# Kernel tuning notes

Hardware: AMD Instinct MI355X
Metric: run time of the kernel (lower is better)

## Reference

```python
import jax, jax.numpy as jnp
import numpy as np


def graph_conv(x, W, b, src, dst, n_nodes):
    """DGL GraphConv, norm='both', activation=relu.
    Pre-scale by out-degree^-1/2 of src, project (in>out so project first),
    sum-aggregate over edges, post-scale by in-degree^-1/2 of dst."""
    ones = jnp.ones(src.shape[0], dtype=x.dtype)
    deg_out = jax.ops.segment_sum(ones, src, num_segments=n_nodes)
    deg_in = jax.ops.segment_sum(ones, dst, num_segments=n_nodes)
    norm_src = jnp.clip(deg_out, 1.0, None) ** -0.5  # [N]
    norm_dst = jnp.clip(deg_in, 1.0, None) ** -0.5   # [N]
    h = x * norm_src[:, None]
    h = h @ W  # project first since in_feats > out_feats
    # message passing: gather src features, scatter-add into dst
    agg = jax.ops.segment_sum(h[src], dst, num_segments=n_nodes)  # [N, out]
    agg = agg * norm_dst[:, None]
    return jax.nn.relu(agg + b)


def setup_inputs() -> dict:
    key = jax.random.key(0)
    ks = jax.random.split(key, 6)
    N, E, D_IN, D_HID = 50000, 800000, 1024, 256
    x = jax.random.normal(ks[0], (N, D_IN), dtype=jnp.float32)
    src = jax.random.randint(ks[1], (E,), 0, N)
    dst = jax.random.randint(ks[2], (E,), 0, N)
    # Glorot-style init for weights
    W1 = jax.random.normal(ks[3], (D_IN, D_HID), dtype=jnp.float32) * (1.0 / np.sqrt(D_IN))
    b1 = jnp.zeros((D_HID,), dtype=jnp.float32)
    W2 = jax.random.normal(ks[4], (D_HID, 1), dtype=jnp.float32) * (1.0 / np.sqrt(D_HID))
    b2 = jnp.zeros((1,), dtype=jnp.float32)
    return {"x": x, "src": src, "dst": dst, "W1": W1, "b1": b1, "W2": W2, "b2": b2, "n_nodes": N}


def reference(x, src, dst, W1, b1, W2, b2, n_nodes):
    h = graph_conv(x, W1, b1, src, dst, n_nodes)   # [N, 256]
    out = graph_conv(h, W2, b2, src, dst, n_nodes)  # [N, 1]
    return out
```

## Files before the change

kernel.cpp:

```cpp
#include <hip/hip_runtime.h>
#include <hip/hip_bf16.h>

typedef __attribute__((ext_vector_type(8))) short bf16x8;
typedef __attribute__((ext_vector_type(4))) float f32x4;

static __device__ __forceinline__ short f2bf(float f) {
    unsigned u = __float_as_uint(f);
    unsigned r = (u + 0x7FFFu + ((u >> 16) & 1u)) >> 16;
    return (short)(unsigned short)r;
}
static __device__ __forceinline__ float bf2f(short s) {
    return __uint_as_float(((unsigned)(unsigned short)s) << 16);
}

static __device__ __forceinline__ void gload16(const void* g, void* l) {
    __builtin_amdgcn_global_load_lds((const __attribute__((address_space(1))) unsigned int*)g,
                                     (__attribute__((address_space(3))) unsigned int*)l, 16, 0, 0);
}

static __device__ __forceinline__ bf16x8 cvt8(const f32x4 lo, const f32x4 hi) {
    __hip_bfloat162 p0 = __float22bfloat162_rn(make_float2(lo[0], lo[1]));
    __hip_bfloat162 p1 = __float22bfloat162_rn(make_float2(lo[2], lo[3]));
    __hip_bfloat162 p2 = __float22bfloat162_rn(make_float2(hi[0], hi[1]));
    __hip_bfloat162 p3 = __float22bfloat162_rn(make_float2(hi[2], hi[3]));
    short2 s0 = *(short2*)&p0, s1 = *(short2*)&p1, s2 = *(short2*)&p2, s3 = *(short2*)&p3;
    bf16x8 r = {s0.x, s0.y, s1.x, s1.y, s2.x, s2.y, s3.x, s3.y};
    return r;
}

__global__ void deg_kernel(const int* __restrict__ src, const int* __restrict__ dst,
                           int* __restrict__ deg_out, int* __restrict__ deg_in, int E) {
    int e = blockIdx.x * blockDim.x + threadIdx.x;
    if (e < E) {
        atomicAdd(&deg_out[src[e]], 1);
        atomicAdd(&deg_in[dst[e]], 1);
    }
}

__global__ void norm_kernel(const int* __restrict__ deg_out, const int* __restrict__ deg_in,
                            float* __restrict__ ns, float* __restrict__ nd, int N) {
    int i = blockIdx.x * blockDim.x + threadIdx.x;
    if (i < N) {
        ns[i] = rsqrtf((float)max(deg_out[i], 1));
        nd[i] = rsqrtf((float)max(deg_in[i], 1));
    }
}

__global__ void scan_part1(const int* __restrict__ deg, int* __restrict__ bsum, int N) {
    __shared__ int red[256];
    int i = blockIdx.x * 256 + threadIdx.x;
    red[threadIdx.x] = (i < N) ? deg[i] : 0;
    __syncthreads();
    for (int off = 128; off > 0; off >>= 1) {
        if (threadIdx.x < off) red[threadIdx.x] += red[threadIdx.x + off];
        __syncthreads();
    }
    if (threadIdx.x == 0) bsum[blockIdx.x] = red[0];
}

__global__ void scan_part2(const int* __restrict__ bsum, int* __restrict__ bsum_ex, int NB,
                           int* __restrict__ offsets, int N, int E) {
    __shared__ int s[256];
    int t = threadIdx.x;
    int v = (t < NB) ? bsum[t] : 0;
    s[t] = v;
    __syncthreads();
    for (int off = 1; off < 256; off <<= 1) {
        int u = (t >= off) ? s[t - off] : 0;
        __syncthreads();
        s[t] += u;
        __syncthreads();
    }
    bsum_ex[t] = s[t] - v;
    if (t == 0) offsets[N] = E;
}

__global__ void scan_part3(const int* __restrict__ deg, const int* __restrict__ bsum_ex,
                           int* __restrict__ offsets, int N) {
    __shared__ int s[256];
    int t = threadIdx.x, i = blockIdx.x * 256 + t;
    int v = (i < N) ? deg[i] : 0;
    s[t] = v;
    __syncthreads();
    for (int off = 1; off < 256; off <<= 1) {
        int u = (t >= off) ? s[t - off] : 0;
        __syncthreads();
        s[t] += u;
        __syncthreads();
    }
    if (i < N) offsets[i] = bsum_ex[blockIdx.x] + s[t] - v;
}

__global__ void scatter_kernel(const int* __restrict__ src, const int* __restrict__ dst,
                               const int* __restrict__ offsets, int* __restrict__ cursor,
                               int* __restrict__ bucket, int E) {
    int e = blockIdx.x * blockDim.x + threadIdx.x;
    if (e < E) {
        int d = dst[e];
        int p = atomicAdd(&cursor[d], 1);
        bucket[offsets[d] + p] = src[e];
    }
}

__global__ __launch_bounds__(1024) void transpose_w1(const float* __restrict__ W1,
                                                     short* __restrict__ Wt) {
    __shared__ short tile[32][33];
    int k0 = blockIdx.x * 32, n0 = blockIdx.y * 32;
    int tx = threadIdx.x & 31, ty = threadIdx.x >> 5;
    tile[ty][tx] = f2bf(W1[(size_t)(k0 + ty) * 256 + (n0 + tx)]);
    __syncthreads();
    Wt[(size_t)(n0 + ty) * 1024 + (k0 + tx)] = tile[tx][ty];
}

#define BM 128
#define BN 128
#define BK 32
#define CSTR 136

union SMem {
    struct {
        float A[BM * BK];
        short B[BN * BK];
    } s;
    short C[BM * CSTR];
};

__global__ __launch_bounds__(256, 3) void gemm1_kernel(const float* __restrict__ x,
                                                       const short* __restrict__ Wt,
                                                       const float* __restrict__ norm_src,
                                                       short* __restrict__ hb, int M) {
    __shared__ __align__(16) SMem sm;
    __shared__ float ns_lds[BM];
    const int tid  = threadIdx.x;
    const int lane = tid & 63;
    const int wave = tid >> 6;
    const int quad = lane >> 4;
    const int mrow = lane & 15;
    const int wm = (wave >> 1) * 64;
    const int wn = (wave & 1) * 64;
    const int bm = blockIdx.x * BM;
    const int bn = blockIdx.y * BN;

    if (tid < BM) ns_lds[tid] = norm_src[min(bm + tid, M - 1)];

    f32x4 acc[4][4] = {};

    const int aL_r = lane >> 3;
    const int aL_c = (lane & 7) ^ (aL_r & 7);
    const int bL_r = lane >> 2;
    const int bL_c = (lane & 3) ^ ((lane >> 3) & 3);

    for (int k0 = 0; k0 < 1024; k0 += BK) {
#pragma unroll
        for (int i = 0; i < 4; i++) {
            int rowbase = wave * 32 + i * 8;
            int r = rowbase + aL_r;
            if (bm + r < M)
                gload16(x + (size_t)(bm + r) * 1024 + k0 + aL_c * 4, &sm.s.A[rowbase * 32]);
        }
#pragma unroll
        for (int i = 0; i < 2; i++) {
            int nbase = wave * 32 + i * 16;
            int n = nbase + bL_r;
            gload16(Wt + (size_t)(bn + n) * 1024 + k0 + bL_c * 8, &sm.s.B[nbase * 32]);
        }
        __syncthreads();

        bf16x8 af[4], bfr[4];
#pragma unroll
        for (int mi = 0; mi < 4; mi++) {
            int row = wm + mi * 16 + mrow;
            f32x4 lo = *(const f32x4*)&sm.s.A[row * 32 + (((quad * 2 + 0) ^ (mrow & 7)) * 4)];
            f32x4 hi = *(const f32x4*)&sm.s.A[row * 32 + (((quad * 2 + 1) ^ (mrow & 7)) * 4)];
            af[mi] = cvt8(lo, hi);
        }
#pragma unroll
        for (int ni = 0; ni < 4; ni++) {
            int n = wn + ni * 16 + mrow;
            bfr[ni] = *(const bf16x8*)&sm.s.B[n * 32 + ((quad ^ ((mrow >> 1) & 3)) * 8)];
        }
#pragma unroll
        for (int mi = 0; mi < 4; mi++)
#pragma unroll
            for (int ni = 0; ni < 4; ni++)
                acc[mi][ni] = __builtin_amdgcn_mfma_f32_16x16x32_bf16(af[mi], bfr[ni], acc[mi][ni], 0, 0, 0);
        __syncthreads();
    }

#pragma unroll
    for (int mi = 0; mi < 4; mi++) {
#pragma unroll
        for (int reg = 0; reg < 4; reg++) {
            int row = wm + mi * 16 + quad * 4 + reg;
            float nsv = ns_lds[row];
#pragma unroll
            for (int ni = 0; ni < 4; ni++) {
                int col = wn + ni * 16 + mrow;
                sm.C[row * CSTR + col] = f2bf(acc[mi][ni][reg] * nsv);
            }
        }
    }
    __syncthreads();
#pragma unroll
    for (int j = 0; j < 8; j++) {
        int row = wave * 4 + (lane >> 4) + j * 16;
        int chunk = lane & 15;
        if (bm + row < M) {
            int4 v = *(const int4*)&sm.C[row * CSTR + chunk * 8];
            *(int4*)(hb + (size_t)(bm + row) * 256 + bn + chunk * 8) = v;
        }
    }
}

__global__ __launch_bounds__(256) void agg1_kernel(const short* __restrict__ hb,
                                                   const int* __restrict__ bucket,
                                                   const int* __restrict__ offsets,
                                                   const float* __restrict__ norm_dst,
                                                   const float* __restrict__ norm_src,
                                                   const float* __restrict__ b1,
                                                   const float* __restrict__ W2,
                                                   float* __restrict__ z, int N) {
    int wave = threadIdx.x >> 6;
    int lane = threadIdx.x & 63;
    int node = blockIdx.x * 4 + wave;
    if (node >= N) return;
    int beg = offsets[node], end = offsets[node + 1];
    float a0 = 0.f, a1 = 0.f, a2 = 0.f, a3 = 0.f;
    int e = beg;
    for (; e + 3 < end; e += 4) {
        int s0 = bucket[e], s1 = bucket[e + 1], s2 = bucket[e + 2], s3 = bucket[e + 3];
        short4 v0 = *(const short4*)(hb + (size_t)s0 * 256 + lane * 4);
        short4 v1 = *(const short4*)(hb + (size_t)s1 * 256 + lane * 4);
        short4 v2 = *(const short4*)(hb + (size_t)s2 * 256 + lane * 4);
        short4 v3 = *(const short4*)(hb + (size_t)s3 * 256 + lane * 4);
        a0 += bf2f(v0.x) + bf2f(v1.x) + bf2f(v2.x) + bf2f(v3.x);
        a1 += bf2f(v0.y) + bf2f(v1.y) + bf2f(v2.y) + bf2f(v3.y);
        a2 += bf2f(v0.z) + bf2f(v1.z) + bf2f(v2.z) + bf2f(v3.z);
        a3 += bf2f(v0.w) + bf2f(v1.w) + bf2f(v2.w) + bf2f(v3.w);
    }
    for (; e < end; e++) {
        short4 v0 = *(const short4*)(hb + (size_t)bucket[e] * 256 + lane * 4);
        a0 += bf2f(v0.x); a1 += bf2f(v0.y); a2 += bf2f(v0.z); a3 += bf2f(v0.w);
    }
    float nd = norm_dst[node];
    float4 bb = *(const float4*)(b1 + lane * 4);
    float o0 = fmaxf(a0 * nd + bb.x, 0.f);
    float o1 = fmaxf(a1 * nd + bb.y, 0.f);
    float o2 = fmaxf(a2 * nd + bb.z, 0.f);
    float o3 = fmaxf(a3 * nd + bb.w, 0.f);
    float4 w = *(const float4*)(W2 + lane * 4);
    float p = o0 * w.x + o1 * w.y + o2 * w.z + o3 * w.w;
#pragma unroll
    for (int off = 32; off > 0; off >>= 1) p += __shfl_xor(p, off, 64);
    if (lane == 0) z[node] = p * norm_src[node];
}

__global__ void agg2_kernel(const float* __restrict__ z, const int* __restrict__ bucket,
                            const int* __restrict__ offsets, const float* __restrict__ norm_dst,
                            const float* __restrict__ b2, float* __restrict__ out, int N) {
    int i = blockIdx.x * blockDim.x + threadIdx.x;
    if (i >= N) return;
    int beg = offsets[i], end = offsets[i + 1];
    float s = 0.f;
    for (int e = beg; e < end; e++) s += z[bucket[e]];
    out[i] = fmaxf(s * norm_dst[i] + b2[0], 0.f);
}

extern "C" void kernel_launch(void* const* d_in, const int* in_sizes, int n_in,
                              void* d_out, int out_size, void* d_ws, size_t ws_size,
                              hipStream_t stream) {
    const int D_HID = in_sizes[4];
    const int D_IN  = in_sizes[3] / D_HID;
    const int N     = in_sizes[0] / D_IN;
    const int E     = in_sizes[1];

    const float* x   = (const float*)d_in[0];
    const int*   src = (const int*)d_in[1];
    const int*   dst = (const int*)d_in[2];
    const float* W1  = (const float*)d_in[3];
    const float* b1  = (const float*)d_in[4];
    const float* W2  = (const float*)d_in[5];
    const float* b2  = (const float*)d_in[6];
    float* out = (float*)d_out;

    char* p = (char*)d_ws;
    auto alloc = [&](size_t bytes) {
        void* r = (void*)p;
        p += (bytes + 255) & ~(size_t)255;
        return r;
    };
    int*   deg_out  = (int*)alloc((size_t)N * 4);
    int*   deg_in   = (int*)alloc((size_t)N * 4);
    int*   cursor   = (int*)alloc((size_t)N * 4);
    float* norm_src = (float*)alloc((size_t)N * 4);
    float* norm_dst = (float*)alloc((size_t)N * 4);
    int*   offsets  = (int*)alloc((size_t)(N + 1) * 4);
    int*   bucket   = (int*)alloc((size_t)E * 4);
    short* Wt       = (short*)alloc((size_t)D_IN * D_HID * 2);
    short* hb       = (short*)alloc((size_t)N * D_HID * 2);
    float* z        = (float*)alloc((size_t)N * 4);
    int*   bsum     = (int*)alloc(256 * 4);
    int*   bsum_ex  = (int*)alloc(256 * 4);

    const int NB = (N + 255) / 256;

    hipMemsetAsync(deg_out, 0, (size_t)N * 4, stream);
    hipMemsetAsync(deg_in,  0, (size_t)N * 4, stream);
    hipMemsetAsync(cursor,  0, (size_t)N * 4, stream);

    deg_kernel<<<(E + 255) / 256, 256, 0, stream>>>(src, dst, deg_out, deg_in, E);
    norm_kernel<<<(N + 255) / 256, 256, 0, stream>>>(deg_out, deg_in, norm_src, norm_dst, N);
    scan_part1<<<NB, 256, 0, stream>>>(deg_in, bsum, N);
    scan_part2<<<1, 256, 0, stream>>>(bsum, bsum_ex, NB, offsets, N, E);
    scan_part3<<<NB, 256, 0, stream>>>(deg_in, bsum_ex, offsets, N);
    scatter_kernel<<<(E + 255) / 256, 256, 0, stream>>>(src, dst, offsets, cursor, bucket, E);
    transpose_w1<<<dim3(D_IN / 32, D_HID / 32), 1024, 0, stream>>>(W1, Wt);
    gemm1_kernel<<<dim3((N + BM - 1) / BM, D_HID / BN), 256, 0, stream>>>(x, Wt, norm_src, hb, N);
    agg1_kernel<<<(N + 3) / 4, 256, 0, stream>>>(hb, bucket, offsets, norm_dst, norm_src, b1, W2, z, N);
    agg2_kernel<<<(N + 255) / 256, 256, 0, stream>>>(z, bucket, offsets, norm_dst, b2, out, N);
}
```

Before: 506.7 us.

## Register-prefetch and pre-convert x to bf16 in LDS, halve GEMM tile, unroll gather

The GEMM now loads x through registers one K-step ahead and converts it to bf16 before writing to LDS, replacing the direct global-to-LDS fp32 copy and the per-wave conversion after each LDS read. This halves A's LDS footprint. The M tile shrinks from 128 to 64 and the occupancy hint rises from 3 to 6 blocks. The aggregation loop unroll goes from 4 to 8 edges so more gathers are in flight. The cost is more blocks, less reuse of B per block, and a swizzle-free LDS layout that may cause bank conflicts.

```diff
diff --git a/kernel.cpp b/kernel.cpp
--- a/kernel.cpp
+++ b/kernel.cpp
@@ -18,11 +18,11 @@
                                      (__attribute__((address_space(3))) unsigned int*)l, 16, 0, 0);
 }
 
-static __device__ __forceinline__ bf16x8 cvt8(const f32x4 lo, const f32x4 hi) {
-    __hip_bfloat162 p0 = __float22bfloat162_rn(make_float2(lo[0], lo[1]));
-    __hip_bfloat162 p1 = __float22bfloat162_rn(make_float2(lo[2], lo[3]));
-    __hip_bfloat162 p2 = __float22bfloat162_rn(make_float2(hi[0], hi[1]));
-    __hip_bfloat162 p3 = __float22bfloat162_rn(make_float2(hi[2], hi[3]));
+static __device__ __forceinline__ bf16x8 cvt8(const float4 lo, const float4 hi) {
+    __hip_bfloat162 p0 = __float22bfloat162_rn(make_float2(lo.x, lo.y));
+    __hip_bfloat162 p1 = __float22bfloat162_rn(make_float2(lo.z, lo.w));
+    __hip_bfloat162 p2 = __float22bfloat162_rn(make_float2(hi.x, hi.y));
+    __hip_bfloat162 p3 = __float22bfloat162_rn(make_float2(hi.z, hi.w));
     short2 s0 = *(short2*)&p0, s1 = *(short2*)&p1, s2 = *(short2*)&p2, s3 = *(short2*)&p3;
     bf16x8 r = {s0.x, s0.y, s1.x, s1.y, s2.x, s2.y, s3.x, s3.y};
     return r;
@@ -112,20 +112,20 @@
     Wt[(size_t)(n0 + ty) * 1024 + (k0 + tx)] = tile[tx][ty];
 }
 
-#define BM 128
+#define BM 64
 #define BN 128
 #define BK 32
 #define CSTR 136
 
 union SMem {
     struct {
-        float A[BM * BK];
+        short A[BM * BK];
         short B[BN * BK];
     } s;
     short C[BM * CSTR];
 };
 
-__global__ __launch_bounds__(256, 3) void gemm1_kernel(const float* __restrict__ x,
+__global__ __launch_bounds__(256, 6) void gemm1_kernel(const float* __restrict__ x,
                                                        const short* __restrict__ Wt,
                                                        const float* __restrict__ norm_src,
                                                        short* __restrict__ hb, int M) {
@@ -136,51 +136,48 @@
     const int wave = tid >> 6;
     const int quad = lane >> 4;
     const int mrow = lane & 15;
-    const int wm = (wave >> 1) * 64;
+    const int wm = (wave >> 1) * 32;
     const int wn = (wave & 1) * 64;
     const int bm = blockIdx.x * BM;
     const int bn = blockIdx.y * BN;
 
     if (tid < BM) ns_lds[tid] = norm_src[min(bm + tid, M - 1)];
 
-    f32x4 acc[4][4] = {};
-
-    const int aL_r = lane >> 3;
-    const int aL_c = (lane & 7) ^ (aL_r & 7);
-    const int bL_r = lane >> 2;
-    const int bL_c = (lane & 3) ^ ((lane >> 3) & 3);
+    f32x4 acc[2][4] = {};
+
+    const int a_row = tid >> 2;
+    const int a_chk = tid & 3;
+    const float* a_src = x + (size_t)min(bm + a_row, M - 1) * 1024 + a_chk * 8;
+    const bool a_ok = (bm + a_row < M);
+
+    float4 a_lo, a_hi;
+    a_lo = a_ok ? *(const float4*)(a_src + 0) : make_float4(0.f, 0.f, 0.f, 0.f);
+    a_hi = a_ok ? *(const float4*)(a_src + 4) : make_float4(0.f, 0.f, 0.f, 0.f);
 
     for (int k0 = 0; k0 < 1024; k0 += BK) {
-#pragma unroll
-        for (int i = 0; i < 4; i++) {
-            int rowbase = wave * 32 + i * 8;
-            int r = rowbase + aL_r;
-            if (bm + r < M)
-                gload16(x + (size_t)(bm + r) * 1024 + k0 + aL_c * 4, &sm.s.A[rowbase * 32]);
-        }
 #pragma unroll
         for (int i = 0; i < 2; i++) {
             int nbase = wave * 32 + i * 16;
-            int n = nbase + bL_r;
-            gload16(Wt + (size_t)(bn + n) * 1024 + k0 + bL_c * 8, &sm.s.B[nbase * 32]);
-        }
-        __syncthreads();
-
-        bf16x8 af[4], bfr[4];
-#pragma unroll
-        for (int mi = 0; mi < 4; mi++) {
-            int row = wm + mi * 16 + mrow;
-            f32x4 lo = *(const f32x4*)&sm.s.A[row * 32 + (((quad * 2 + 0) ^ (mrow & 7)) * 4)];
-            f32x4 hi = *(const f32x4*)&sm.s.A[row * 32 + (((quad * 2 + 1) ^ (mrow & 7)) * 4)];
-            af[mi] = cvt8(lo, hi);
-        }
-#pragma unroll
-        for (int ni = 0; ni < 4; ni++) {
-            int n = wn + ni * 16 + mrow;
-            bfr[ni] = *(const bf16x8*)&sm.s.B[n * 32 + ((quad ^ ((mrow >> 1) & 3)) * 8)];
-        }
-#pragma unroll
-        for (int mi = 0; mi < 4; mi++)
+            int n = nbase + (lane >> 2);
+            gload16(Wt + (size_t)(bn + n) * 1024 + k0 + (lane & 3) * 8, &sm.s.B[nbase * 32]);
+        }
+        *(bf16x8*)&sm.s.A[a_row * 32 + a_chk * 8] = cvt8(a_lo, a_hi);
+        __syncthreads();
+
+        if (k0 + BK < 1024) {
+            a_lo = a_ok ? *(const float4*)(a_src + k0 + BK + 0) : make_float4(0.f, 0.f, 0.f, 0.f);
+            a_hi = a_ok ? *(const float4*)(a_src + k0 + BK + 4) : make_float4(0.f, 0.f, 0.f, 0.f);
+        }
+
+        bf16x8 af[2], bfr[4];
+#pragma unroll
+        for (int mi = 0; mi < 2; mi++)
+            af[mi] = *(const bf16x8*)&sm.s.A[(wm + mi * 16 + mrow) * 32 + quad * 8];
+#pragma unroll
+        for (int ni = 0; ni < 4; ni++)
+            bfr[ni] = *(const bf16x8*)&sm.s.B[(wn + ni * 16 + mrow) * 32 + quad * 8];
+#pragma unroll
+        for (int mi = 0; mi < 2; mi++)
 #pragma unroll
             for (int ni = 0; ni < 4; ni++)
                 acc[mi][ni] = __builtin_amdgcn_mfma_f32_16x16x32_bf16(af[mi], bfr[ni], acc[mi][ni], 0, 0, 0);
@@ -188,7 +185,7 @@
     }
 
 #pragma unroll
-    for (int mi = 0; mi < 4; mi++) {
+    for (int mi = 0; mi < 2; mi++) {
 #pragma unroll
         for (int reg = 0; reg < 4; reg++) {
             int row = wm + mi * 16 + quad * 4 + reg;
@@ -202,9 +199,9 @@
     }
     __syncthreads();
 #pragma unroll
-    for (int j = 0; j < 8; j++) {
-        int row = wave * 4 + (lane >> 4) + j * 16;
-        int chunk = lane & 15;
+    for (int j = 0; j < 4; j++) {
+        int row = (tid >> 4) + j * 16;
+        int chunk = tid & 15;
         if (bm + row < M) {
             int4 v = *(const int4*)&sm.C[row * CSTR + chunk * 8];
             *(int4*)(hb + (size_t)(bm + row) * 256 + bn + chunk * 8) = v;
@@ -227,16 +224,16 @@
     int beg = offsets[node], end = offsets[node + 1];
     float a0 = 0.f, a1 = 0.f, a2 = 0.f, a3 = 0.f;
     int e = beg;
-    for (; e + 3 < end; e += 4) {
-        int s0 = bucket[e], s1 = bucket[e + 1], s2 = bucket[e + 2], s3 = bucket[e + 3];
-        short4 v0 = *(const short4*)(hb + (size_t)s0 * 256 + lane * 4);
-        short4 v1 = *(const short4*)(hb + (size_t)s1 * 256 + lane * 4);
-        short4 v2 = *(const short4*)(hb + (size_t)s2 * 256 + lane * 4);
-        short4 v3 = *(const short4*)(hb + (size_t)s3 * 256 + lane * 4);
-        a0 += bf2f(v0.x) + bf2f(v1.x) + bf2f(v2.x) + bf2f(v3.x);
-        a1 += bf2f(v0.y) + bf2f(v1.y) + bf2f(v2.y) + bf2f(v3.y);
-        a2 += bf2f(v0.z) + bf2f(v1.z) + bf2f(v2.z) + bf2f(v3.z);
-        a3 += bf2f(v0.w) + bf2f(v1.w) + bf2f(v2.w) + bf2f(v3.w);
+    for (; e + 7 < end; e += 8) {
+        short4 v[8];
+#pragma unroll
+        for (int j = 0; j < 8; j++)
+            v[j] = *(const short4*)(hb + (size_t)bucket[e + j] * 256 + lane * 4);
+#pragma unroll
+        for (int j = 0; j < 8; j++) {
+            a0 += bf2f(v[j].x); a1 += bf2f(v[j].y);
+            a2 += bf2f(v[j].z); a3 += bf2f(v[j].w);
+        }
     }
     for (; e < end; e++) {
         short4 v0 = *(const short4*)(hb + (size_t)bucket[e] * 256 + lane * 4);
```

Result: slower. 526.2 us (+3.8%).
